# Kernel optimization log

Measured on AMD Instinct MI355X. Metric: run time of the kernel, lower is better.

The kernel has to match this reference:

```python
import jax, jax.numpy as jnp
import numpy as np

B, S, D, H, M, E, K = 4, 2048, 1024, 2048, 64, 8, 2  # batch, seq, d_model, max_neurons, moe_hidden, experts, top_k


def setup_inputs() -> dict:
    key = jax.random.key(0)
    ks = jax.random.split(key, 10)
    r = lambda k, shape: jax.random.normal(k, shape, dtype=jnp.float32) * 0.02
    return {
        "inputs_embeds": jax.random.normal(ks[0], (B, S, D), dtype=jnp.float32),
        "enc_W": r(ks[1], (D, H)), "enc_b": jnp.zeros((H,), jnp.float32),
        "s2c_W": r(ks[2], (H, M)), "s2c_b": jnp.zeros((M,), jnp.float32),
        "rW1": r(ks[3], (M, 64)), "rb1": jnp.zeros((64,), jnp.float32),
        "rW2": r(ks[4], (64, E)), "rb2": jnp.zeros((E,), jnp.float32),
        "We1": r(ks[5], (E, M, H // 2)), "be1": jnp.zeros((E, H // 2), jnp.float32),
        "We2": r(ks[6], (E, H // 2, M)), "be2": jnp.zeros((E, M), jnp.float32),
        "c2s_W": r(ks[7], (M, H)), "c2s_b": jnp.zeros((H,), jnp.float32),
        "dec_W": r(ks[8], (H, D)), "dec_b": jnp.zeros((D,), jnp.float32),
        "ln_g": jnp.ones((D,), jnp.float32), "ln_b": jnp.zeros((D,), jnp.float32),
    }


def _layernorm(x, g, b, eps=1e-5):
    mu = x.mean(-1, keepdims=True)
    var = ((x - mu) ** 2).mean(-1, keepdims=True)
    return (x - mu) * jax.lax.rsqrt(var + eps) * g + b


def _forward(inputs_embeds, enc_W, enc_b, s2c_W, s2c_b, rW1, rb1, rW2, rb2,
             We1, be1, We2, be2, c2s_W, c2s_b, dec_W, dec_b, ln_g, ln_b):
    b, s, _ = inputs_embeds.shape
    # GIFNeuron encoder (rate-coded surrogate spikes)
    spikes_enc = jax.nn.sigmoid(inputs_embeds @ enc_W + enc_b)          # (B,S,H)
    flat = spikes_enc.reshape(b * s, H)                                  # (N,H)
    # SpikeToContinuousBridge ('rate'): projection to MoE hidden
    cont = flat @ s2c_W + s2c_b                                          # (N,M)
    # LiquidMoERouter: 2-layer router, softmax, top-k, renormalize
    logits = jnp.tanh(cont @ rW1 + rb1) @ rW2 + rb2                      # (N,E)
    probs = jax.nn.softmax(logits, axis=-1)
    topw, topi = jax.lax.top_k(probs, K)                                 # (N,K)
    w = topw / topw.sum(-1, keepdims=True)
    # dense per-token per-expert gate == sum_k weights[:,k] * (indices[:,k]==e)
    gates = (jax.nn.one_hot(topi, E, dtype=cont.dtype) * w[..., None]).sum(1)  # (N,E)
    # SNNExpert MLP per expert, dense dispatch + weighted combine (index_add equivalent)
    h = jax.nn.relu(jnp.einsum('nm,emh->enh', cont, We1) + be1[:, None, :])    # (E,N,H/2)
    expert_out = jnp.einsum('enh,ehm->enm', h, We2) + be2[:, None, :]          # (E,N,M)
    output_flat = jnp.einsum('enm,ne->nm', expert_out, gates)                  # (N,M)
    # ContinuousToSpikeBridge ('poisson', expected rate), 2D -> 1 timestep
    spikes_moe = jax.nn.sigmoid(output_flat @ c2s_W + c2s_b).reshape(b, s, H)
    # GIFNeuron decoder + LayerNorm
    decoded = jax.nn.sigmoid(spikes_moe @ dec_W + dec_b)                 # (B,S,D)
    return _layernorm(decoded, ln_g, ln_b)


def reference(inputs_embeds, enc_W, enc_b, s2c_W, s2c_b, rW1, rb1, rW2, rb2,
              We1, be1, We2, be2, c2s_W, c2s_b, dec_W, dec_b, ln_g, ln_b):
    return _forward(inputs_embeds, enc_W, enc_b, s2c_W, s2c_b, rW1, rb1, rW2, rb2,
                    We1, be1, We2, be2, c2s_W, c2s_b, dec_W, dec_b, ln_g, ln_b)
```

## Files before the change

kernel.cpp:

```cpp
#include <hip/hip_runtime.h>
#include <hip/hip_bf16.h>
#include <cstdint>
#include <cstddef>

#define TOK    8192
#define DMODEL 1024
#define HDIM   2048
#define MDIM   64
#define NEXP   8
#define HHALF  1024

using f32x4  = __attribute__((ext_vector_type(4))) float;
using bf16x8 = __attribute__((ext_vector_type(8))) __bf16;
using bf16x4 = __attribute__((ext_vector_type(4))) __bf16;

__device__ __forceinline__ void async16(const void* g, void* l) {
  __builtin_amdgcn_global_load_lds(
      (const __attribute__((address_space(1))) unsigned int*)g,
      (__attribute__((address_space(3))) unsigned int*)l, 16, 0, 0);
}

__global__ __launch_bounds__(256) void preamble_kernel(
    const float* __restrict__ X, __bf16* __restrict__ Xb,
    const float* __restrict__ encW, __bf16* __restrict__ encWT,
    const float* __restrict__ s2cW, __bf16* __restrict__ s2cWT,
    const float* __restrict__ c2sW, __bf16* __restrict__ c2sWT,
    const float* __restrict__ decW, __bf16* __restrict__ decWT,
    const float* __restrict__ We1, __bf16* __restrict__ We1T,
    const float* __restrict__ We2, __bf16* __restrict__ We2T) {
  __shared__ float ts[32][33];
  const int tid = threadIdx.x;
  int b = blockIdx.x;
  if (b < 8192) {
    int i = b * 256 + tid;
    float4 v = ((const float4*)X)[i];
    bf16x4 o = { (__bf16)v.x, (__bf16)v.y, (__bf16)v.z, (__bf16)v.w };
    ((bf16x4*)Xb)[i] = o;
    return;
  }
  b -= 8192;
  const float* in; __bf16* outp; int R, C, tx, ty;
  if (b < 2048)              { in = encW; outp = encWT; R = 1024; C = 2048; tx = b % 64; ty = b / 64; }
  else if ((b -= 2048) < 128){ in = s2cW; outp = s2cWT; R = 2048; C = 64;   tx = b % 2;  ty = b / 2;  }
  else if ((b -= 128) < 128) { in = c2sW; outp = c2sWT; R = 64;   C = 2048; tx = b % 64; ty = b / 64; }
  else if ((b -= 128) < 2048){ in = decW; outp = decWT; R = 2048; C = 1024; tx = b % 32; ty = b / 32; }
  else if ((b -= 2048) < 512){ int s = b / 64, t = b % 64;
                               in = We1 + (size_t)s * 65536; outp = We1T + (size_t)s * 65536;
                               R = 64; C = 1024; tx = t % 32; ty = t / 32; }
  else                       { b -= 512; int s = b / 64, t = b % 64;
                               in = We2 + (size_t)s * 65536; outp = We2T + (size_t)s * 65536;
                               R = 1024; C = 64; tx = t % 2; ty = t / 2; }
  const int c0 = tx * 32, r0 = ty * 32;
  const int x = tid & 31, y = tid >> 5;
  #pragma unroll
  for (int i = y; i < 32; i += 8) ts[i][x] = in[(size_t)(r0 + i) * C + c0 + x];
  __syncthreads();
  #pragma unroll
  for (int i = y; i < 32; i += 8)
    outp[(size_t)(c0 + i) * R + r0 + x] = (__bf16)ts[x][i];
}
#define PREAMBLE_BLOCKS (8192 + 2048 + 128 + 128 + 2048 + 512 + 512)

template <int BM, int BN, int OUT_BF16, int ACT, int BIAS, int SUMA>
__global__ __launch_bounds__(256) void gemm_bt(
    const __bf16* __restrict__ A, const __bf16* __restrict__ Bt,
    const float* __restrict__ bias, void* __restrict__ Cout,
    int M, int N, int K, const __bf16* __restrict__ A2) {
  constexpr int BK = 64;
  constexpr int WTM = BM / 32;
  constexpr int WTN = BN / 32;
  constexpr int NBUF = SUMA ? 1 : 2;
  __shared__ __bf16 As[NBUF * BM * BK];
  __shared__ __bf16 Bs[NBUF * BN * BK];
  const int tid = threadIdx.x;
  const int wave = tid >> 6, lane = tid & 63;
  const int quad = lane >> 4, l16 = lane & 15;
  const int m0 = blockIdx.x * BM, n0 = blockIdx.y * BN;
  const int ks = K / gridDim.z;
  const int kbeg = blockIdx.z * ks;
  const int wm = (wave & 1) * (BM / 2);
  const int wn = (wave >> 1) * (BN / 2);
  const int lrow = lane >> 3;
  const int lchunk = lane & 7;
  constexpr int A_ISSUES = BM / 32;
  constexpr int B_ISSUES = BN / 32;
  f32x4 acc[WTM][WTN] = {};

  const __bf16* aSrc[A_ISSUES];
  const __bf16* bSrc[B_ISSUES];
  #pragma unroll
  for (int t = 0; t < A_ISSUES; ++t) {
    int row = (t * 4 + wave) * 8 + lrow;
    aSrc[t] = A + (size_t)(m0 + row) * K + kbeg + (lchunk ^ (row & 7)) * 8;
  }
  #pragma unroll
  for (int t = 0; t < B_ISSUES; ++t) {
    int row = (t * 4 + wave) * 8 + lrow;
    bSrc[t] = Bt + (size_t)(n0 + row) * K + kbeg + (lchunk ^ (row & 7)) * 8;
  }
  int aOff[WTM][2], bOff[WTN][2];
  #pragma unroll
  for (int i = 0; i < WTM; ++i) {
    int row = wm + i * 16 + l16;
    #pragma unroll
    for (int kk = 0; kk < 2; ++kk)
      aOff[i][kk] = row * BK + (((kk * 4 + quad) ^ (row & 7)) * 8);
  }
  #pragma unroll
  for (int j = 0; j < WTN; ++j) {
    int row = wn + j * 16 + l16;
    #pragma unroll
    for (int kk = 0; kk < 2; ++kk)
      bOff[j][kk] = row * BK + (((kk * 4 + quad) ^ (row & 7)) * 8);
  }

  auto stage = [&](__bf16* Ad, __bf16* Bd) {
    #pragma unroll
    for (int t = 0; t < A_ISSUES; ++t) {
      async16(aSrc[t], Ad + (t * 4 + wave) * 8 * BK);
      aSrc[t] += BK;
    }
    #pragma unroll
    for (int t = 0; t < B_ISSUES; ++t) {
      async16(bSrc[t], Bd + (t * 4 + wave) * 8 * BK);
      bSrc[t] += BK;
    }
  };
  auto compute = [&](const __bf16* Ab, const __bf16* Bb) {
    #pragma unroll
    for (int kk = 0; kk < 2; ++kk) {
      bf16x8 af[WTM], bfr[WTN];
      #pragma unroll
      for (int i = 0; i < WTM; ++i) af[i] = *(const bf16x8*)(Ab + aOff[i][kk]);
      #pragma unroll
      for (int j = 0; j < WTN; ++j) bfr[j] = *(const bf16x8*)(Bb + bOff[j][kk]);
      #pragma unroll
      for (int i = 0; i < WTM; ++i)
        #pragma unroll
        for (int j = 0; j < WTN; ++j)
          acc[i][j] = __builtin_amdgcn_mfma_f32_16x16x32_bf16(af[i], bfr[j], acc[i][j], 0, 0, 0);
    }
  };

  const int niter = ks / BK;
  if constexpr (SUMA) {
    for (int it = 0; it < niter; ++it) {
      __syncthreads();
      #pragma unroll
      for (int t = 0; t < A_ISSUES; ++t) {
        int row = (t * 4 + wave) * 8 + lrow;
        size_t go = (size_t)(m0 + row) * K + kbeg + it * BK + lchunk * 8;
        bf16x8 a0 = *(const bf16x8*)(A + go);
        bf16x8 a1 = *(const bf16x8*)(A2 + go);
        bf16x8 s;
        #pragma unroll
        for (int q = 0; q < 8; ++q) s[q] = (__bf16)((float)a0[q] + (float)a1[q]);
        *(bf16x8*)(As + row * BK + ((lchunk ^ (row & 7)) * 8)) = s;
      }
      #pragma unroll
      for (int t = 0; t < B_ISSUES; ++t) {
        async16(bSrc[t], Bs + (t * 4 + wave) * 8 * BK);
        bSrc[t] += BK;
      }
      __syncthreads();
      compute(As, Bs);
    }
  } else {
    __bf16* curA = As;  __bf16* nxtA = As + BM * BK;
    __bf16* curB = Bs;  __bf16* nxtB = Bs + BN * BK;
    stage(curA, curB);
    asm volatile("s_waitcnt vmcnt(0)" ::: "memory");
    __builtin_amdgcn_s_barrier();
    for (int it = 0; it < niter - 1; ++it) {
      stage(nxtA, nxtB);
      compute(curA, curB);
      asm volatile("s_waitcnt vmcnt(0)" ::: "memory");
      __builtin_amdgcn_s_barrier();
      { __bf16* t = curA; curA = nxtA; nxtA = t; }
      { __bf16* t = curB; curB = nxtB; nxtB = t; }
    }
    compute(curA, curB);
  }

  char* Cz = (char*)Cout + (size_t)blockIdx.z * M * N * (OUT_BF16 ? 2 : 4);
  #pragma unroll
  for (int i = 0; i < WTM; ++i)
    #pragma unroll
    for (int j = 0; j < WTN; ++j)
      #pragma unroll
      for (int r = 0; r < 4; ++r) {
        int m = m0 + wm + i * 16 + quad * 4 + r;
        int n = n0 + wn + j * 16 + l16;
        float v = acc[i][j][r];
        if (BIAS) v += bias[n];
        if (ACT == 1) v = 1.0f / (1.0f + __expf(-v));
        if (OUT_BF16)
          ((__bf16*)Cz)[(size_t)m * N + n] = (__bf16)v;
        else
          ((float*)Cz)[(size_t)m * N + n] = v;
      }
}

__global__ __launch_bounds__(256) void router_kernel(
    const float* __restrict__ contP, const float* __restrict__ s2c_b,
    const float* __restrict__ rW1, const float* __restrict__ rb1,
    const float* __restrict__ rW2, const float* __restrict__ rb2,
    __bf16* __restrict__ contB, int* __restrict__ e01,
    float2* __restrict__ g01) {
  const int wave = threadIdx.x >> 6, lane = threadIdx.x & 63;
  const int n = blockIdx.x * 4 + wave;
  const size_t base = (size_t)n * 64 + lane;
  const size_t slab = (size_t)TOK * 64;
  float c = contP[base] + contP[base + slab] + contP[base + 2 * slab] +
            contP[base + 3 * slab] + s2c_b[lane];
  contB[base] = (__bf16)c;
  float acc = rb1[lane];
  #pragma unroll
  for (int i = 0; i < 64; ++i) {
    float ci = __shfl(c, i);
    acc = fmaf(ci, rW1[i * 64 + lane], acc);
  }
  float t = tanhf(acc);
  float logit[8];
  #pragma unroll
  for (int e = 0; e < 8; ++e) {
    float v = t * rW2[lane * 8 + e];
    #pragma unroll
    for (int o = 32; o; o >>= 1) v += __shfl_xor(v, o);
    logit[e] = v + rb2[e];
  }
  float mx = logit[0];
  #pragma unroll
  for (int e = 1; e < 8; ++e) mx = fmaxf(mx, logit[e]);
  float p[8];
  #pragma unroll
  for (int e = 0; e < 8; ++e) p[e] = __expf(logit[e] - mx);
  float v0 = p[0]; int e0 = 0;
  #pragma unroll
  for (int e = 1; e < 8; ++e) if (p[e] > v0) { v0 = p[e]; e0 = e; }
  float v1 = -1.0f; int e1 = 0;
  #pragma unroll
  for (int e = 0; e < 8; ++e) if (e != e0 && p[e] > v1) { v1 = p[e]; e1 = e; }
  float inv = 1.0f / (v0 + v1);
  if (lane == 0) {
    e01[n] = e0 | (e1 << 8);
    g01[n] = make_float2(v0 * inv, v1 * inv);
  }
}

__global__ __launch_bounds__(256) void moe_fused_kernel(
    const __bf16* __restrict__ contB, const __bf16* __restrict__ We1T,
    const __bf16* __restrict__ We2T, const float* __restrict__ be1,
    const float* __restrict__ be2, const int* __restrict__ e01,
    const float2* __restrict__ g01, __bf16* __restrict__ slab0,
    __bf16* __restrict__ slab1) {
  constexpr int TT = 128;
  const int e = blockIdx.y;
  const int t0 = blockIdx.x * TT;
  __shared__ __bf16 cont_s[TT * 64];
  __shared__ __bf16 w1_s[64 * 64];
  __shared__ __bf16 w2_s[64 * 64];
  __shared__ __bf16 h_s[TT * 64];
  __shared__ int   e01_s[TT];
  __shared__ float g0_s[TT], g1_s[TT];
  const int tid = threadIdx.x;
  const int wave = tid >> 6, lane = tid & 63;
  const int quad = lane >> 4, l16 = lane & 15;
  if (tid < TT) {
    e01_s[tid] = e01[t0 + tid];
    float2 g = g01[t0 + tid];
    g0_s[tid] = g.x; g1_s[tid] = g.y;
  }
  for (int i = tid; i < TT * 8; i += 256) {
    int r = i >> 3, cc = i & 7;
    *(uint4*)(cont_s + r * 64 + ((cc ^ (r & 7)) * 8)) =
        *(const uint4*)(contB + (size_t)(t0 + r) * 64 + cc * 8);
  }
  const int wtok = wave * 32;
  f32x4 acc2[2][4] = {};
  for (int hc = 0; hc < HHALF; hc += 64) {
    __syncthreads();
    for (int c = tid; c < 512; c += 256) {
      int r = c >> 3, cc = c & 7;
      *(uint4*)(w1_s + r * 64 + ((cc ^ (r & 7)) * 8)) =
          *(const uint4*)(We1T + ((size_t)e * HHALF + hc + r) * 64 + cc * 8);
      *(uint4*)(w2_s + r * 64 + ((cc ^ (r & 7)) * 8)) =
          *(const uint4*)(We2T + ((size_t)e * 64 + r) * HHALF + hc + cc * 8);
    }
    __syncthreads();
    f32x4 acc1[2][4] = {};
    #pragma unroll
    for (int kk = 0; kk < 2; ++kk) {
      bf16x8 af[2], bfr[4];
      #pragma unroll
      for (int i = 0; i < 2; ++i) {
        int row = wtok + i * 16 + l16;
        af[i] = *(const bf16x8*)(cont_s + row * 64 + (((kk * 4 + quad) ^ (row & 7)) * 8));
      }
      #pragma unroll
      for (int j = 0; j < 4; ++j) {
        int row = j * 16 + l16;
        bfr[j] = *(const bf16x8*)(w1_s + row * 64 + (((kk * 4 + quad) ^ (row & 7)) * 8));
      }
      #pragma unroll
      for (int i = 0; i < 2; ++i)
        #pragma unroll
        for (int j = 0; j < 4; ++j)
          acc1[i][j] = __builtin_amdgcn_mfma_f32_16x16x32_bf16(af[i], bfr[j], acc1[i][j], 0, 0, 0);
    }
    #pragma unroll
    for (int i = 0; i < 2; ++i)
      #pragma unroll
      for (int j = 0; j < 4; ++j)
        #pragma unroll
        for (int r = 0; r < 4; ++r) {
          int tr = wtok + i * 16 + quad * 4 + r;
          int hcol = j * 16 + l16;
          float v = acc1[i][j][r] + be1[e * HHALF + hc + hcol];
          h_s[tr * 64 + (((hcol >> 3) ^ (tr & 7)) * 8) + (hcol & 7)] =
              (__bf16)fmaxf(v, 0.0f);
        }
    #pragma unroll
    for (int kk = 0; kk < 2; ++kk) {
      bf16x8 af[2], bfr[4];
      #pragma unroll
      for (int i = 0; i < 2; ++i) {
        int row = wtok + i * 16 + l16;
        af[i] = *(const bf16x8*)(h_s + row * 64 + (((kk * 4 + quad) ^ (row & 7)) * 8));
      }
      #pragma unroll
      for (int j = 0; j < 4; ++j) {
        int row = j * 16 + l16;
        bfr[j] = *(const bf16x8*)(w2_s + row * 64 + (((kk * 4 + quad) ^ (row & 7)) * 8));
      }
      #pragma unroll
      for (int i = 0; i < 2; ++i)
        #pragma unroll
        for (int j = 0; j < 4; ++j)
          acc2[i][j] = __builtin_amdgcn_mfma_f32_16x16x32_bf16(af[i], bfr[j], acc2[i][j], 0, 0, 0);
    }
  }
  #pragma unroll
  for (int i = 0; i < 2; ++i)
    #pragma unroll
    for (int j = 0; j < 4; ++j)
      #pragma unroll
      for (int r = 0; r < 4; ++r) {
        int tr = wtok + i * 16 + quad * 4 + r;
        int m = j * 16 + l16;
        int pe = e01_s[tr];
        size_t o = (size_t)(t0 + tr) * 64 + m;
        if ((pe & 0xff) == e)
          slab0[o] = (__bf16)(g0_s[tr] * (acc2[i][j][r] + be2[e * 64 + m]));
        else if (((pe >> 8) & 0xff) == e)
          slab1[o] = (__bf16)(g1_s[tr] * (acc2[i][j][r] + be2[e * 64 + m]));
      }
}

__global__ __launch_bounds__(256) void ln_kernel(
    const float* __restrict__ x, const float* __restrict__ g,
    const float* __restrict__ b, float* __restrict__ out) {
  const int row = blockIdx.x;
  const float4 v = ((const float4*)(x + (size_t)row * 1024))[threadIdx.x];
  float s1 = v.x + v.y + v.z + v.w;
  float s2 = v.x * v.x + v.y * v.y + v.z * v.z + v.w * v.w;
  #pragma unroll
  for (int o = 32; o; o >>= 1) { s1 += __shfl_xor(s1, o); s2 += __shfl_xor(s2, o); }
  __shared__ float ws1[4], ws2[4];
  const int wave = threadIdx.x >> 6, lane = threadIdx.x & 63;
  if (lane == 0) { ws1[wave] = s1; ws2[wave] = s2; }
  __syncthreads();
  s1 = ws1[0] + ws1[1] + ws1[2] + ws1[3];
  s2 = ws2[0] + ws2[1] + ws2[2] + ws2[3];
  const float mu = s1 * (1.0f / 1024.0f);
  const float var = s2 * (1.0f / 1024.0f) - mu * mu;
  const float inv = rsqrtf(var + 1e-5f);
  const int col = threadIdx.x * 4;
  const float4 gv = *(const float4*)(g + col);
  const float4 bv = *(const float4*)(b + col);
  float4 o;
  o.x = (v.x - mu) * inv * gv.x + bv.x;
  o.y = (v.y - mu) * inv * gv.y + bv.y;
  o.z = (v.z - mu) * inv * gv.z + bv.z;
  o.w = (v.w - mu) * inv * gv.w + bv.w;
  *(float4*)(out + (size_t)row * 1024 + col) = o;
}

extern "C" void kernel_launch(void* const* d_in, const int* in_sizes, int n_in,
                              void* d_out, int out_size, void* d_ws, size_t ws_size,
                              hipStream_t stream) {
  const float* X     = (const float*)d_in[0];
  const float* enc_W = (const float*)d_in[1];
  const float* enc_b = (const float*)d_in[2];
  const float* s2c_W = (const float*)d_in[3];
  const float* s2c_b = (const float*)d_in[4];
  const float* rW1   = (const float*)d_in[5];
  const float* rb1   = (const float*)d_in[6];
  const float* rW2   = (const float*)d_in[7];
  const float* rb2   = (const float*)d_in[8];
  const float* We1   = (const float*)d_in[9];
  const float* be1   = (const float*)d_in[10];
  const float* We2   = (const float*)d_in[11];
  const float* be2   = (const float*)d_in[12];
  const float* c2s_W = (const float*)d_in[13];
  const float* c2s_b = (const float*)d_in[14];
  const float* dec_W = (const float*)d_in[15];
  const float* dec_b = (const float*)d_in[16];
  const float* ln_g  = (const float*)d_in[17];
  const float* ln_b  = (const float*)d_in[18];
  float* out = (float*)d_out;

  char* ws = (char*)d_ws;
  size_t off = 0;
  auto take = [&](size_t bytes) -> char* {
    char* p = ws + off;
    off = (off + bytes + 255) & ~(size_t)255;
    return p;
  };
  const size_t SLAB = (size_t)TOK * HDIM * 2;
  char*   slabA     = take(SLAB);
  char*   slabB     = take(SLAB);
  __bf16* encWT     = (__bf16*)take((size_t)HDIM * DMODEL * 2);
  __bf16* s2cWT     = (__bf16*)take((size_t)MDIM * HDIM * 2);
  __bf16* c2sWT     = (__bf16*)take((size_t)HDIM * MDIM * 2);
  __bf16* decWT     = (__bf16*)take((size_t)DMODEL * HDIM * 2);
  __bf16* We1T      = (__bf16*)take((size_t)NEXP * HHALF * MDIM * 2);
  __bf16* We2T      = (__bf16*)take((size_t)NEXP * MDIM * HHALF * 2);
  __bf16* contB     = (__bf16*)take((size_t)TOK * MDIM * 2);
  int*    e01       = (int*)take((size_t)TOK * 4);
  float2* g01       = (float2*)take((size_t)TOK * 8);
  __bf16* oslab0    = (__bf16*)take((size_t)TOK * MDIM * 2);
  __bf16* oslab1    = (__bf16*)take((size_t)TOK * MDIM * 2);
  if (off > ws_size) return;

  __bf16* Xb        = (__bf16*)slabA;
  float*  contP     = (float*)(slabA + (size_t)TOK * DMODEL * 2);
  __bf16* spikesMoe = (__bf16*)slabA;
  __bf16* spikesEnc = (__bf16*)slabB;
  float*  decoded   = (float*)slabB;

  preamble_kernel<<<PREAMBLE_BLOCKS, 256, 0, stream>>>(
      X, Xb, enc_W, encWT, s2c_W, s2cWT, c2s_W, c2sWT, dec_W, decWT,
      We1, We1T, We2, We2T);

  gemm_bt<128, 128, 1, 1, 1, 0><<<dim3(TOK / 128, HDIM / 128, 1), 256, 0, stream>>>(
      Xb, encWT, enc_b, spikesEnc, TOK, HDIM, DMODEL, nullptr);
  gemm_bt<128, 64, 0, 0, 0, 0><<<dim3(TOK / 128, 1, 4), 256, 0, stream>>>(
      spikesEnc, s2cWT, nullptr, contP, TOK, MDIM, HDIM, nullptr);
  router_kernel<<<TOK / 4, 256, 0, stream>>>(contP, s2c_b, rW1, rb1, rW2, rb2,
                                             contB, e01, g01);
  moe_fused_kernel<<<dim3(TOK / 128, NEXP), 256, 0, stream>>>(
      contB, We1T, We2T, be1, be2, e01, g01, oslab0, oslab1);
  gemm_bt<128, 128, 1, 1, 1, 1><<<dim3(TOK / 128, HDIM / 128, 1), 256, 0, stream>>>(
      oslab0, c2sWT, c2s_b, spikesMoe, TOK, HDIM, MDIM, oslab1);
  gemm_bt<128, 128, 0, 1, 1, 0><<<dim3(TOK / 128, DMODEL / 128, 1), 256, 0, stream>>>(
      spikesMoe, decWT, dec_b, decoded, TOK, DMODEL, HDIM, nullptr);
  ln_kernel<<<TOK, 256, 0, stream>>>(decoded, ln_g, ln_b, out);
}
```

Measured before the change: 314.4 us.

## Triple-buffer GEMM pipeline and use 8-wave 128x256 tiles for large GEMMs

The bf16 MFMA GEMM now uses three LDS stages with a partial vmcnt wait, so two tiles of loads are in flight while one is computed. It also takes a wave-count template parameter, and the encoder and decoder GEMMs move to 128x256 tiles on 512-thread blocks. The aim is to hide global-load latency better and raise the reuse of each loaded tile. In exchange, LDS use grows to 3x48KB per block, which may limit occupancy, and the hardcoded vmcnt(6) ties the pipeline to exactly six loads per stage.

```diff
diff --git a/kernel.cpp b/kernel.cpp
--- a/kernel.cpp
+++ b/kernel.cpp
@@ -19,6 +19,8 @@
       (const __attribute__((address_space(1))) unsigned int*)g,
       (__attribute__((address_space(3))) unsigned int*)l, 16, 0, 0);
 }
+__device__ __forceinline__ void wait_vm6() { asm volatile("s_waitcnt vmcnt(6)" ::: "memory"); }
+__device__ __forceinline__ void wait_vm0() { asm volatile("s_waitcnt vmcnt(0)" ::: "memory"); }
 
 __global__ __launch_bounds__(256) void preamble_kernel(
     const float* __restrict__ X, __bf16* __restrict__ Xb,
@@ -61,15 +63,19 @@
 }
 #define PREAMBLE_BLOCKS (8192 + 2048 + 128 + 128 + 2048 + 512 + 512)
 
-template <int BM, int BN, int OUT_BF16, int ACT, int BIAS, int SUMA>
-__global__ __launch_bounds__(256) void gemm_bt(
+template <int BM, int BN, int WAVES, int OUT_BF16, int ACT, int BIAS, int SUMA>
+__global__ __launch_bounds__(WAVES * 64) void gemm_bt(
     const __bf16* __restrict__ A, const __bf16* __restrict__ Bt,
     const float* __restrict__ bias, void* __restrict__ Cout,
     int M, int N, int K, const __bf16* __restrict__ A2) {
   constexpr int BK = 64;
+  constexpr int WAVES_N = WAVES / 2;
   constexpr int WTM = BM / 32;
-  constexpr int WTN = BN / 32;
-  constexpr int NBUF = SUMA ? 1 : 2;
+  constexpr int WTN = BN / (WAVES_N * 16);
+  constexpr int NBUF = SUMA ? 1 : 3;
+  constexpr int A_ISSUES = BM / (8 * WAVES);
+  constexpr int B_ISSUES = BN / (8 * WAVES);
+  static_assert(SUMA || (A_ISSUES + B_ISSUES == 6), "vmcnt literal assumes 6 loads/stage");
   __shared__ __bf16 As[NBUF * BM * BK];
   __shared__ __bf16 Bs[NBUF * BN * BK];
   const int tid = threadIdx.x;
@@ -79,23 +85,21 @@
   const int ks = K / gridDim.z;
   const int kbeg = blockIdx.z * ks;
   const int wm = (wave & 1) * (BM / 2);
-  const int wn = (wave >> 1) * (BN / 2);
+  const int wn = (wave >> 1) * (BN / WAVES_N);
   const int lrow = lane >> 3;
   const int lchunk = lane & 7;
-  constexpr int A_ISSUES = BM / 32;
-  constexpr int B_ISSUES = BN / 32;
   f32x4 acc[WTM][WTN] = {};
 
   const __bf16* aSrc[A_ISSUES];
   const __bf16* bSrc[B_ISSUES];
   #pragma unroll
   for (int t = 0; t < A_ISSUES; ++t) {
-    int row = (t * 4 + wave) * 8 + lrow;
+    int row = (t * WAVES + wave) * 8 + lrow;
     aSrc[t] = A + (size_t)(m0 + row) * K + kbeg + (lchunk ^ (row & 7)) * 8;
   }
   #pragma unroll
   for (int t = 0; t < B_ISSUES; ++t) {
-    int row = (t * 4 + wave) * 8 + lrow;
+    int row = (t * WAVES + wave) * 8 + lrow;
     bSrc[t] = Bt + (size_t)(n0 + row) * K + kbeg + (lchunk ^ (row & 7)) * 8;
   }
   int aOff[WTM][2], bOff[WTN][2];
@@ -117,12 +121,12 @@
   auto stage = [&](__bf16* Ad, __bf16* Bd) {
     #pragma unroll
     for (int t = 0; t < A_ISSUES; ++t) {
-      async16(aSrc[t], Ad + (t * 4 + wave) * 8 * BK);
+      async16(aSrc[t], Ad + (t * WAVES + wave) * 8 * BK);
       aSrc[t] += BK;
     }
     #pragma unroll
     for (int t = 0; t < B_ISSUES; ++t) {
-      async16(bSrc[t], Bd + (t * 4 + wave) * 8 * BK);
+      async16(bSrc[t], Bd + (t * WAVES + wave) * 8 * BK);
       bSrc[t] += BK;
     }
   };
@@ -148,7 +152,7 @@
       __syncthreads();
       #pragma unroll
       for (int t = 0; t < A_ISSUES; ++t) {
-        int row = (t * 4 + wave) * 8 + lrow;
+        int row = (t * WAVES + wave) * 8 + lrow;
         size_t go = (size_t)(m0 + row) * K + kbeg + it * BK + lchunk * 8;
         bf16x8 a0 = *(const bf16x8*)(A + go);
         bf16x8 a1 = *(const bf16x8*)(A2 + go);
@@ -159,27 +163,26 @@
       }
       #pragma unroll
       for (int t = 0; t < B_ISSUES; ++t) {
-        async16(bSrc[t], Bs + (t * 4 + wave) * 8 * BK);
+        async16(bSrc[t], Bs + (t * WAVES + wave) * 8 * BK);
         bSrc[t] += BK;
       }
       __syncthreads();
       compute(As, Bs);
     }
   } else {
-    __bf16* curA = As;  __bf16* nxtA = As + BM * BK;
-    __bf16* curB = Bs;  __bf16* nxtB = Bs + BN * BK;
-    stage(curA, curB);
-    asm volatile("s_waitcnt vmcnt(0)" ::: "memory");
-    __builtin_amdgcn_s_barrier();
-    for (int it = 0; it < niter - 1; ++it) {
-      stage(nxtA, nxtB);
-      compute(curA, curB);
-      asm volatile("s_waitcnt vmcnt(0)" ::: "memory");
+    __bf16* a0 = As;  __bf16* a1 = As + BM * BK;  __bf16* a2 = As + 2 * BM * BK;
+    __bf16* b0 = Bs;  __bf16* b1 = Bs + BN * BK;  __bf16* b2 = Bs + 2 * BN * BK;
+    stage(a0, b0);
+    if (niter > 1) stage(a1, b1);
+    for (int it = 0; it < niter; ++it) {
+      if (it + 1 < niter) wait_vm6(); else wait_vm0();
       __builtin_amdgcn_s_barrier();
-      { __bf16* t = curA; curA = nxtA; nxtA = t; }
-      { __bf16* t = curB; curB = nxtB; nxtB = t; }
-    }
-    compute(curA, curB);
+      if (it + 2 < niter) stage(a2, b2);
+      compute(a0, b0);
+      __bf16* t;
+      t = a0; a0 = a1; a1 = a2; a2 = t;
+      t = b0; b0 = b1; b1 = b2; b2 = t;
+    }
   }
 
   char* Cz = (char*)Cout + (size_t)blockIdx.z * M * N * (OUT_BF16 ? 2 : 4);
@@ -443,17 +446,17 @@
       X, Xb, enc_W, encWT, s2c_W, s2cWT, c2s_W, c2sWT, dec_W, decWT,
       We1, We1T, We2, We2T);
 
-  gemm_bt<128, 128, 1, 1, 1, 0><<<dim3(TOK / 128, HDIM / 128, 1), 256, 0, stream>>>(
+  gemm_bt<128, 256, 8, 1, 1, 1, 0><<<dim3(TOK / 128, HDIM / 256, 1), 512, 0, stream>>>(
       Xb, encWT, enc_b, spikesEnc, TOK, HDIM, DMODEL, nullptr);
-  gemm_bt<128, 64, 0, 0, 0, 0><<<dim3(TOK / 128, 1, 4), 256, 0, stream>>>(
+  gemm_bt<128, 64, 4, 0, 0, 0, 0><<<dim3(TOK / 128, 1, 4), 256, 0, stream>>>(
       spikesEnc, s2cWT, nullptr, contP, TOK, MDIM, HDIM, nullptr);
   router_kernel<<<TOK / 4, 256, 0, stream>>>(contP, s2c_b, rW1, rb1, rW2, rb2,
                                              contB, e01, g01);
   moe_fused_kernel<<<dim3(TOK / 128, NEXP), 256, 0, stream>>>(
       contB, We1T, We2T, be1, be2, e01, g01, oslab0, oslab1);
-  gemm_bt<128, 128, 1, 1, 1, 1><<<dim3(TOK / 128, HDIM / 128, 1), 256, 0, stream>>>(
+  gemm_bt<128, 128, 4, 1, 1, 1, 1><<<dim3(TOK / 128, HDIM / 128, 1), 256, 0, stream>>>(
       oslab0, c2sWT, c2s_b, spikesMoe, TOK, HDIM, MDIM, oslab1);
-  gemm_bt<128, 128, 0, 1, 1, 0><<<dim3(TOK / 128, DMODEL / 128, 1), 256, 0, stream>>>(
+  gemm_bt<128, 256, 8, 0, 1, 1, 0><<<dim3(TOK / 128, DMODEL / 256, 1), 512, 0, stream>>>(
       spikesMoe, decWT, dec_b, decoded, TOK, DMODEL, HDIM, nullptr);
   ln_kernel<<<TOK, 256, 0, stream>>>(decoded, ln_g, ln_b, out);
 }
```

New measurement: 322.8 us. 2.7% more time.
